# Performance work log

Hardware: AMD Instinct MI355X
Metric: run time of the kernel (lower is better)

Reference implementation:

```python
import jax, jax.numpy as jnp
import numpy as np

MAX_SEQ = 768  # hardcoded in original compute_freqs_cis
THETA = 10000.0


def _freqs_cis(C, T):
    # freqs over FULL embed dim C (matches original, not per-head)
    freqs = 1.0 / THETA ** (jnp.arange(0, C, 2, dtype=jnp.float32)[: C // 2] / C)
    t = jnp.arange(MAX_SEQ, dtype=jnp.float32)
    ang = jnp.outer(t, freqs)  # [MAX_SEQ, C/2]
    return jnp.cos(ang)[:T], jnp.sin(ang)[:T]  # each [T, C/2]


def _apply_rope(u):
    # u: [B, T, C]; rotate adjacent channel pairs across full C
    B, T, C = u.shape
    fr, fi = _freqs_cis(C, T)           # [T, C/2]
    u2 = u.astype(jnp.float32).reshape(B, T, C // 2, 2)
    ur, ui = u2[..., 0], u2[..., 1]     # [B, T, C/2]
    out_r = ur * fr - ui * fi
    out_i = ur * fi + ui * fr
    return jnp.stack([out_r, out_i], axis=-1).reshape(B, T, C).astype(u.dtype)


def setup_inputs() -> dict:
    key = jax.random.key(0)
    k1, k2, k3 = jax.random.split(key, 3)
    B, T, C = 16, 768, 1024
    x = jax.random.normal(k1, (B, T, C), dtype=jnp.float32)
    Wqkv = jax.random.normal(k2, (3 * C, C), dtype=jnp.float32) * 0.02
    bqkv = jnp.zeros((3 * C,), dtype=jnp.float32)
    Wo = jax.random.normal(k3, (C, C), dtype=jnp.float32) * 0.02
    bo = jnp.zeros((C,), dtype=jnp.float32)
    return {"x": x, "Wqkv": Wqkv, "bqkv": bqkv, "Wo": Wo, "bo": bo}


def reference(x, Wqkv, bqkv, Wo, bo):
    B, T, C = x.shape
    H = 16
    D = C // H
    qkv = x @ Wqkv.T + bqkv                      # [B, T, 3C]
    q, k, v = jnp.split(qkv, 3, axis=-1)
    q = _apply_rope(q)
    k = _apply_rope(k)
    # [B, H, T, D]
    q = q.reshape(B, T, H, D).transpose(0, 2, 1, 3)
    k = k.reshape(B, T, H, D).transpose(0, 2, 1, 3)
    v = v.reshape(B, T, H, D).transpose(0, 2, 1, 3)
    scale = 1.0 / jnp.sqrt(jnp.asarray(D, dtype=q.dtype))
    scores = jnp.einsum("bhqd,bhkd->bhqk", q, k) * scale
    causal = jnp.tril(jnp.ones((T, T), dtype=bool))
    scores = jnp.where(causal, scores, jnp.finfo(scores.dtype).min)
    attn = jax.nn.softmax(scores, axis=-1)
    y = jnp.einsum("bhqk,bhkd->bhqd", attn, v)   # [B, H, T, D]
    y = y.transpose(0, 2, 1, 3).reshape(B, T, C)
    return y @ Wo.T + bo
```

## Files before the change

### kernel.cpp

```cpp
#include <hip/hip_runtime.h>
#include <hip/hip_bf16.h>

typedef __attribute__((ext_vector_type(8))) short bf16x8;
typedef __attribute__((ext_vector_type(4))) float f32x4;
typedef unsigned short u16;
typedef unsigned int u32;

#define DEV __device__ __forceinline__

DEV float bf2f(u16 v) { u32 u = ((u32)v) << 16; return __builtin_bit_cast(float, u); }
DEV u16 f2bf(float f) {
    u32 u = __builtin_bit_cast(u32, f);
    u32 r = (u + 0x7FFFu + ((u >> 16) & 1u)) >> 16;
    return (u16)r;
}
DEV u16 f2bf_trunc(float f) { return (u16)(__builtin_bit_cast(u32, f) >> 16); }

DEV void gll16(const u16* g, u16* l) {
    __builtin_amdgcn_global_load_lds((const __attribute__((address_space(1))) void*)g,
                                     (__attribute__((address_space(3))) void*)l, 16, 0, 0);
}

#define WAIT_VM0()   asm volatile("s_waitcnt vmcnt(0)" ::: "memory")
#define WAIT_LGKM0() asm volatile("s_waitcnt lgkmcnt(0)" ::: "memory")
#define BAR()        __builtin_amdgcn_s_barrier()
#define BARF()       asm volatile("s_barrier" ::: "memory")

__global__ void detect_kernel(const u32* __restrict__ x, int* __restrict__ flag) {
    __shared__ int cnt;
    if (threadIdx.x == 0) cnt = 0;
    __syncthreads();
    int c = 0;
    for (int i = threadIdx.x; i < 4096; i += 256) {
        u32 w = x[i];
        u32 e = (w >> 7) & 0xFF;
        c += (e >= 110 && e <= 132) ? 1 : 0;
    }
    atomicAdd(&cnt, c);
    __syncthreads();
    if (threadIdx.x == 0) *flag = (cnt * 2 > 4096) ? 1 : 0;
}

DEV void cvt8(const void* in, u16* out, int i, int fl) {
    if (fl) {
        ((bf16x8*)out)[i] = ((const bf16x8*)in)[i];
    } else {
        float4 a = ((const float4*)in)[2 * i], b = ((const float4*)in)[2 * i + 1];
        bf16x8 o;
        o[0] = (short)f2bf(a.x); o[1] = (short)f2bf(a.y);
        o[2] = (short)f2bf(a.z); o[3] = (short)f2bf(a.w);
        o[4] = (short)f2bf(b.x); o[5] = (short)f2bf(b.y);
        o[6] = (short)f2bf(b.z); o[7] = (short)f2bf(b.w);
        ((bf16x8*)out)[i] = o;
    }
}

__global__ void prep_kernel(const void* __restrict__ x, u16* __restrict__ xb,
                            const void* __restrict__ Wq, u16* __restrict__ Wqb,
                            const void* __restrict__ Wo, u16* __restrict__ Wob,
                            float2* __restrict__ tab, const int* __restrict__ flag) {
    constexpr int N8X = 1572864, N8W = 393216, N8O = 131072;
    constexpr int C1 = N8X, C2 = N8X + N8W, C3 = N8X + N8W + N8O;
    constexpr int TOTAL = C3 + 768 * 512;
    const int fl = *flag;
    const int stride = gridDim.x * 256;
    for (int i = blockIdx.x * 256 + threadIdx.x; i < TOTAL; i += stride) {
        if (i < C1)       cvt8(x, xb, i, fl);
        else if (i < C2)  cvt8(Wq, Wqb, i - C1, fl);
        else if (i < C3)  cvt8(Wo, Wob, i - C2, fl);
        else {
            int r = i - C3;
            int t = r >> 9, j = r & 511;
            float freq = expf(-(float)(2 * j) * (9.210340371976184f / 1024.0f));
            float ang = (float)t * freq;
            tab[r] = make_float2(cosf(ang), sinf(ang));
        }
    }
}

template<int BN>
__global__ __launch_bounds__(512, 2)
void gemm256p_kernel(const u16* __restrict__ A, const u16* __restrict__ W,
                     const void* __restrict__ bias, void* __restrict__ C,
                     int N, const int* __restrict__ flag, int out_mode,
                     const float2* __restrict__ tab, int rope) {
    constexpr int K = 1024, NT = 16;
    constexpr int NF = BN / 64;
    __shared__ u16 lds[2][16384 + BN * 64];
    const int tid = threadIdx.x;
    const int l = tid & 63, w = tid >> 6;
    const int wm = w >> 2, wn = w & 3;
    const int lo = l & 15, hi = l >> 4;

    const int M0 = blockIdx.x * 256, N0 = blockIdx.y * BN;

    const int rS = tid >> 3;
    const int qS = (tid & 7) ^ (rS & 7);
    const u16* Ag = A + (size_t)(M0 + rS) * K + qS * 8;
    const u16* Wg = W + (size_t)(N0 + rS) * K + qS * 8;
    const int lb = w * 512;

    f32x4 acc[8][NF] = {};

#define STG_A(kt, slot, half)                                                  \
    {                                                                          \
        u16* sA_ = &lds[slot][(half) * 8192];                                  \
        const u16* ga_ = Ag + (kt) * 64 + (size_t)(128 * (half)) * K;          \
        gll16(ga_,                  sA_ + lb);                                 \
        gll16(ga_ + (size_t)64 * K, sA_ + 4096 + lb);                          \
    }
#define STG_B(kt, slot, half)                                                  \
    {                                                                          \
        u16* sB_ = &lds[slot][16384 + (half) * 8192];                          \
        const u16* gb_ = Wg + (kt) * 64 + (size_t)(128 * (half)) * K;          \
        gll16(gb_,                  sB_ + lb);                                 \
        gll16(gb_ + (size_t)64 * K, sB_ + 4096 + lb);                          \
    }
#define STG_B_ALL(kt, slot)                                                    \
    { STG_B(kt, slot, 0); if (BN == 256) STG_B(kt, slot, 1); }

    STG_A(0, 0, 0); STG_A(0, 0, 1);
    STG_B_ALL(0, 0);
    WAIT_VM0();
    BARF();

    const int csw = lo & 7;

#pragma unroll 1
    for (int t = 0; t < NT; ++t) {
        const int cur = t & 1, nxt = cur ^ 1;
        const u16* sA = &lds[cur][0];
        const u16* sB = &lds[cur][16384];
        bf16x8 afr[4], bfr[NF];

#pragma unroll
        for (int n = 0; n < NF; ++n)
            bfr[n] = *(const bf16x8*)&sB[(wn * (BN / 4) + n * 16 + lo) * 64 + ((hi ^ csw) * 8)];
#pragma unroll
        for (int m = 0; m < 4; ++m)
            afr[m] = *(const bf16x8*)&sA[(wm * 128 + m * 16 + lo) * 64 + ((hi ^ csw) * 8)];
        if (t + 1 < NT) { STG_A(t + 1, nxt, 0); STG_A(t + 1, nxt, 1); }
        BARF();
        __builtin_amdgcn_s_setprio(1);
#pragma unroll
        for (int m = 0; m < 4; ++m)
#pragma unroll
            for (int n = 0; n < NF; ++n)
                acc[m][n] = __builtin_amdgcn_mfma_f32_16x16x32_bf16(afr[m], bfr[n], acc[m][n], 0, 0, 0);
        __builtin_amdgcn_s_setprio(0);
        BARF();

#pragma unroll
        for (int m = 0; m < 4; ++m)
            afr[m] = *(const bf16x8*)&sA[(wm * 128 + 64 + m * 16 + lo) * 64 + ((hi ^ csw) * 8)];
        if (t + 1 < NT) { STG_B_ALL(t + 1, nxt); }
        BARF();
        __builtin_amdgcn_s_setprio(1);
#pragma unroll
        for (int m = 0; m < 4; ++m)
#pragma unroll
            for (int n = 0; n < NF; ++n)
                acc[4 + m][n] = __builtin_amdgcn_mfma_f32_16x16x32_bf16(afr[m], bfr[n], acc[4 + m][n], 0, 0, 0);
        __builtin_amdgcn_s_setprio(0);
        BARF();

#pragma unroll
        for (int n = 0; n < NF; ++n)
            bfr[n] = *(const bf16x8*)&sB[(wn * (BN / 4) + n * 16 + lo) * 64 + (((4 + hi) ^ csw) * 8)];
#pragma unroll
        for (int m = 0; m < 4; ++m)
            afr[m] = *(const bf16x8*)&sA[(wm * 128 + m * 16 + lo) * 64 + (((4 + hi) ^ csw) * 8)];
        BARF();
        __builtin_amdgcn_s_setprio(1);
#pragma unroll
        for (int m = 0; m < 4; ++m)
#pragma unroll
            for (int n = 0; n < NF; ++n)
                acc[m][n] = __builtin_amdgcn_mfma_f32_16x16x32_bf16(afr[m], bfr[n], acc[m][n], 0, 0, 0);
        __builtin_amdgcn_s_setprio(0);
        BARF();

#pragma unroll
        for (int m = 0; m < 4; ++m)
            afr[m] = *(const bf16x8*)&sA[(wm * 128 + 64 + m * 16 + lo) * 64 + (((4 + hi) ^ csw) * 8)];
        WAIT_VM0();
        BARF();
        __builtin_amdgcn_s_setprio(1);
#pragma unroll
        for (int m = 0; m < 4; ++m)
#pragma unroll
            for (int n = 0; n < NF; ++n)
                acc[4 + m][n] = __builtin_amdgcn_mfma_f32_16x16x32_bf16(afr[m], bfr[n], acc[4 + m][n], 0, 0, 0);
        __builtin_amdgcn_s_setprio(0);
        BARF();
    }
#undef STG_A
#undef STG_B
#undef STG_B_ALL

    const int fl = *flag;
    const int f32out = out_mode ? (fl == 0) : 0;
    const int do_rope = rope && (N0 < 2048);
#pragma unroll
    for (int mi = 0; mi < 8; ++mi) {
        const int rbase = M0 + wm * 128 + (mi >> 2) * 64 + (mi & 3) * 16 + hi * 4;
        const int tbase = (M0 % 768) + wm * 128 + (mi >> 2) * 64 + (mi & 3) * 16 + hi * 4;
#pragma unroll
        for (int n = 0; n < NF; ++n) {
            const int col = N0 + wn * (BN / 4) + lo + n * 16;
            float bi = fl ? bf2f(((const u16*)bias)[col]) : ((const float*)bias)[col];
            const int jf = (col & 1023) >> 1;
            const int odd = col & 1;
#pragma unroll
            for (int j = 0; j < 4; ++j) {
                float v = acc[mi][n][j] + bi;
                if (do_rope) {
                    float partner = __shfl_xor(v, 1);
                    float2 cs = tab[(tbase + j) * 512 + jf];
                    v = odd ? (v * cs.x + partner * cs.y) : (v * cs.x - partner * cs.y);
                }
                size_t idx = (size_t)(rbase + j) * N + col;
                if (f32out) ((float*)C)[idx] = v;
                else        ((u16*)C)[idx] = f2bf(v);
            }
        }
    }
}

__global__ __launch_bounds__(512)
void attn_kernel(const u16* __restrict__ qkv, u16* __restrict__ y) {
    constexpr int T = 768, CH = 1024, QKVC = 3072;
    constexpr float NEG = -30000.0f;
    __shared__ u16 Ks[2][64 * 64];
    __shared__ u16 Vt[64 * 72];
    __shared__ u16 Ps[128 * 72];

    const int tid = threadIdx.x, l = tid & 63, w = tid >> 6;
    const int qt = blockIdx.x, h = blockIdx.y, b = blockIdx.z;
    const int lo = l & 15, hi = l >> 4;
    const int kk = hi * 8;
    const int swzk = (lo & 7) * 8;

    const int qrow = qt * 128 + w * 16 + lo;
    const u16* qptr = qkv + (size_t)(b * T + qrow) * QKVC + h * 64 + kk;
    bf16x8 aq0r = *(const bf16x8*)qptr;
    bf16x8 aq1r = *(const bf16x8*)(qptr + 32);
    bf16x8 aq0, aq1;
#pragma unroll
    for (int e = 0; e < 8; ++e) {
        aq0[e] = (short)f2bf(bf2f((u16)aq0r[e]) * 0.125f);
        aq1[e] = (short)f2bf(bf2f((u16)aq1r[e]) * 0.125f);
    }

    f32x4 o[4] = {};
    float mrun[4] = {NEG, NEG, NEG, NEG};
    float lrun[4] = {0.f, 0.f, 0.f, 0.f};

    const int ksr = w * 8 + (l >> 3);
    const int ksc = ((l & 7) ^ ((l >> 3) & 7)) * 8;
    const u16* kbase = qkv + (size_t)(b * T + ksr) * QKVC + CH + h * 64 + ksc;

    const int vd0 = (tid & 7) * 8;
    const int vswz = (tid & 7) * 8;
    const int vr0 = tid >> 3;
    const u16* vbase = qkv + (size_t)(b * T) * QKVC + 2 * CH + h * 64 + vd0;

    const int NTk = 2 * qt + 2;

    gll16(kbase, &Ks[0][w * 512]);
    bf16x8 cv0 = *(const bf16x8*)(vbase + (size_t)vr0 * QKVC);
    WAIT_VM0();
#pragma unroll
    for (int e = 0; e < 8; ++e)
        Vt[(vd0 + e) * 72 + (vr0 ^ vswz)] = (u16)cv0[e];

    for (int kt = 0; kt < NTk; ++kt) {
        const int cur = kt & 1, nxt = cur ^ 1;
        bf16x8 nv0;
        if (kt + 1 < NTk) {
            const size_t koff = (size_t)((kt + 1) * 64) * QKVC;
            gll16(kbase + koff, &Ks[nxt][w * 512]);
            nv0 = *(const bf16x8*)(vbase + (size_t)((kt + 1) * 64 + vr0) * QKVC);
        }
        WAIT_LGKM0();
        BAR();

        __builtin_amdgcn_s_setprio(1);
        f32x4 s[4];
#pragma unroll
        for (int n = 0; n < 4; ++n) {
            bf16x8 kb0 = *(const bf16x8*)&Ks[cur][(n * 16 + lo) * 64 + (kk ^ swzk)];
            bf16x8 kb1 = *(const bf16x8*)&Ks[cur][(n * 16 + lo) * 64 + ((32 + kk) ^ swzk)];
            f32x4 z = {0.f, 0.f, 0.f, 0.f};
            z = __builtin_amdgcn_mfma_f32_16x16x32_bf16(aq0, kb0, z, 0, 0, 0);
            z = __builtin_amdgcn_mfma_f32_16x16x32_bf16(aq1, kb1, z, 0, 0, 0);
            s[n] = z;
        }
        __builtin_amdgcn_s_setprio(0);

        if (kt >= 2 * qt) {
#pragma unroll
            for (int n = 0; n < 4; ++n) {
                int kcol = kt * 64 + n * 16 + lo;
#pragma unroll
                for (int j = 0; j < 4; ++j)
                    if (kcol > qt * 128 + w * 16 + hi * 4 + j) s[n][j] = NEG;
            }
        }
        float mx[4];
#pragma unroll
        for (int j = 0; j < 4; ++j) {
            float m0 = fmaxf(fmaxf(s[0][j], s[1][j]), fmaxf(s[2][j], s[3][j]));
            m0 = fmaxf(m0, __shfl_xor(m0, 1));
            m0 = fmaxf(m0, __shfl_xor(m0, 2));
            m0 = fmaxf(m0, __shfl_xor(m0, 4));
            m0 = fmaxf(m0, __shfl_xor(m0, 8));
            mx[j] = m0;
        }
        float g = fmaxf(fmaxf(mx[0] - mrun[0], mx[1] - mrun[1]),
                        fmaxf(mx[2] - mrun[2], mx[3] - mrun[3]));
        if (!__all(g <= 8.0f)) {
#pragma unroll
            for (int j = 0; j < 4; ++j) {
                float mn = fmaxf(mrun[j], mx[j]);
                float c = __expf(mrun[j] - mn);
                mrun[j] = mn;
                lrun[j] *= c;
#pragma unroll
                for (int n = 0; n < 4; ++n) o[n][j] *= c;
            }
        }
        float p[4][4];
#pragma unroll
        for (int n = 0; n < 4; ++n)
#pragma unroll
            for (int j = 0; j < 4; ++j) {
                p[n][j] = __expf(s[n][j] - mrun[j]);
                Ps[(w * 16 + hi * 4 + j) * 72 + n * 16 + lo] = f2bf_trunc(p[n][j]);
            }
#pragma unroll
        for (int j = 0; j < 4; ++j)
            lrun[j] += p[0][j] + p[1][j] + p[2][j] + p[3][j];

        __builtin_amdgcn_s_setprio(1);
#pragma unroll
        for (int c = 0; c < 2; ++c) {
            bf16x8 pa = *(const bf16x8*)&Ps[(w * 16 + lo) * 72 + c * 32 + kk];
#pragma unroll
            for (int n = 0; n < 4; ++n) {
                const int v = (n * 2 + (lo >> 3)) & 7;
                bf16x8 vb = *(const bf16x8*)&Vt[(n * 16 + lo) * 72 + ((c * 32 + kk) ^ (v * 8))];
                o[n] = __builtin_amdgcn_mfma_f32_16x16x32_bf16(pa, vb, o[n], 0, 0, 0);
            }
        }
        __builtin_amdgcn_s_setprio(0);

        if (kt + 1 < NTk) {
            WAIT_VM0();
            BAR();
#pragma unroll
            for (int e = 0; e < 8; ++e)
                Vt[(vd0 + e) * 72 + (vr0 ^ vswz)] = (u16)nv0[e];
        }
    }

    float inv[4];
#pragma unroll
    for (int j = 0; j < 4; ++j) {
        float r = lrun[j];
        r += __shfl_xor(r, 1);
        r += __shfl_xor(r, 2);
        r += __shfl_xor(r, 4);
        r += __shfl_xor(r, 8);
        inv[j] = (r > 0.f) ? 1.0f / r : 0.f;
    }
#pragma unroll
    for (int n = 0; n < 4; ++n)
#pragma unroll
        for (int j = 0; j < 4; ++j) {
            int t = qt * 128 + w * 16 + hi * 4 + j;
            y[(size_t)(b * T + t) * CH + h * 64 + n * 16 + lo] = f2bf(o[n][j] * inv[j]);
        }
}

extern "C" void kernel_launch(void* const* d_in, const int* in_sizes, int n_in,
                              void* d_out, int out_size, void* d_ws, size_t ws_size,
                              hipStream_t stream) {
    char* ws = (char*)d_ws;
    int*   flag  = (int*)ws;
    u16*   xb    = (u16*)(ws + 256);
    u16*   Wqb   = (u16*)(ws + 256 + 25165824);
    u16*   Wob   = (u16*)(ws + 256 + 31457280);
    u16*   qkv   = (u16*)(ws + 256 + 33570816);
    u16*   y     = (u16*)(ws + 256 + 109068288);
    float2* tab  = (float2*)(ws + 256 + 134234112);

    detect_kernel<<<1, 256, 0, stream>>>((const u32*)d_in[0], flag);
    prep_kernel<<<2048, 256, 0, stream>>>(d_in[0], xb, d_in[1], Wqb, d_in[3], Wob, tab, flag);

    gemm256p_kernel<256><<<dim3(48, 12), 512, 0, stream>>>(xb, Wqb, d_in[2], qkv, 3072, flag, 0, tab, 1);
    attn_kernel<<<dim3(6, 16, 16), 512, 0, stream>>>(qkv, y);
    gemm256p_kernel<128><<<dim3(48, 8), 512, 0, stream>>>(y, Wob, d_in[4], d_out, 1024, flag, 1, tab, 0);
}
```

Measured before the change: 294.7 us.

## Halve GEMM K-tile to 32 with smaller LDS and fold dtype detection into prep

The GEMM K-step tile drops from 64 to 32. That halves the LDS footprint per stage, possibly allowing more resident blocks, but doubles the number of pipeline iterations and barriers. The staging loads, the swizzle pattern and the per-iteration schedule are rewritten to match, with one fused stage and a wait before the second MFMA half. The separate dtype-detection kernel is also removed: every prep block now recomputes the detection flag itself, saving one launch at the cost of redundant reads.

Result: no change. 295.2 us (+0.2%).

```diff
diff --git a/kernel.cpp b/kernel.cpp
--- a/kernel.cpp
+++ b/kernel.cpp
@@ -25,21 +25,6 @@
 #define WAIT_LGKM0() asm volatile("s_waitcnt lgkmcnt(0)" ::: "memory")
 #define BAR()        __builtin_amdgcn_s_barrier()
 #define BARF()       asm volatile("s_barrier" ::: "memory")
-
-__global__ void detect_kernel(const u32* __restrict__ x, int* __restrict__ flag) {
-    __shared__ int cnt;
-    if (threadIdx.x == 0) cnt = 0;
-    __syncthreads();
-    int c = 0;
-    for (int i = threadIdx.x; i < 4096; i += 256) {
-        u32 w = x[i];
-        u32 e = (w >> 7) & 0xFF;
-        c += (e >= 110 && e <= 132) ? 1 : 0;
-    }
-    atomicAdd(&cnt, c);
-    __syncthreads();
-    if (threadIdx.x == 0) *flag = (cnt * 2 > 4096) ? 1 : 0;
-}
 
 DEV void cvt8(const void* in, u16* out, int i, int fl) {
     if (fl) {
@@ -58,11 +43,26 @@
 __global__ void prep_kernel(const void* __restrict__ x, u16* __restrict__ xb,
                             const void* __restrict__ Wq, u16* __restrict__ Wqb,
                             const void* __restrict__ Wo, u16* __restrict__ Wob,
-                            float2* __restrict__ tab, const int* __restrict__ flag) {
+                            float2* __restrict__ tab, int* __restrict__ flag) {
+    __shared__ int cnt;
+    if (threadIdx.x == 0) cnt = 0;
+    __syncthreads();
+    {
+        int c = 0;
+        for (int i = threadIdx.x; i < 4096; i += 256) {
+            u32 w = ((const u32*)x)[i];
+            u32 e = (w >> 7) & 0xFF;
+            c += (e >= 110 && e <= 132) ? 1 : 0;
+        }
+        atomicAdd(&cnt, c);
+    }
+    __syncthreads();
+    const int fl = (cnt * 2 > 4096) ? 1 : 0;
+    if (blockIdx.x == 0 && threadIdx.x == 0) *flag = fl;
+
     constexpr int N8X = 1572864, N8W = 393216, N8O = 131072;
     constexpr int C1 = N8X, C2 = N8X + N8W, C3 = N8X + N8W + N8O;
     constexpr int TOTAL = C3 + 768 * 512;
-    const int fl = *flag;
     const int stride = gridDim.x * 256;
     for (int i = blockIdx.x * 256 + threadIdx.x; i < TOTAL; i += stride) {
         if (i < C1)       cvt8(x, xb, i, fl);
@@ -84,9 +84,9 @@
                      const void* __restrict__ bias, void* __restrict__ C,
                      int N, const int* __restrict__ flag, int out_mode,
                      const float2* __restrict__ tab, int rope) {
-    constexpr int K = 1024, NT = 16;
+    constexpr int K = 1024, NT = 32;
     constexpr int NF = BN / 64;
-    __shared__ u16 lds[2][16384 + BN * 64];
+    __shared__ u16 lds[2][8192 + BN * 32];
     const int tid = threadIdx.x;
     const int l = tid & 63, w = tid >> 6;
     const int wm = w >> 2, wn = w & 3;
@@ -94,52 +94,46 @@
 
     const int M0 = blockIdx.x * 256, N0 = blockIdx.y * BN;
 
-    const int rS = tid >> 3;
-    const int qS = (tid & 7) ^ (rS & 7);
+    const int rS = tid >> 2;
+    const int qS = (tid & 3) ^ ((tid >> 3) & 3);
     const u16* Ag = A + (size_t)(M0 + rS) * K + qS * 8;
     const u16* Wg = W + (size_t)(N0 + rS) * K + qS * 8;
     const int lb = w * 512;
 
     f32x4 acc[8][NF] = {};
 
-#define STG_A(kt, slot, half)                                                  \
+#define STAGE(kt, slot)                                                        \
     {                                                                          \
-        u16* sA_ = &lds[slot][(half) * 8192];                                  \
-        const u16* ga_ = Ag + (kt) * 64 + (size_t)(128 * (half)) * K;          \
-        gll16(ga_,                  sA_ + lb);                                 \
-        gll16(ga_ + (size_t)64 * K, sA_ + 4096 + lb);                          \
-    }
-#define STG_B(kt, slot, half)                                                  \
-    {                                                                          \
-        u16* sB_ = &lds[slot][16384 + (half) * 8192];                          \
-        const u16* gb_ = Wg + (kt) * 64 + (size_t)(128 * (half)) * K;          \
-        gll16(gb_,                  sB_ + lb);                                 \
-        gll16(gb_ + (size_t)64 * K, sB_ + 4096 + lb);                          \
-    }
-#define STG_B_ALL(kt, slot)                                                    \
-    { STG_B(kt, slot, 0); if (BN == 256) STG_B(kt, slot, 1); }
-
-    STG_A(0, 0, 0); STG_A(0, 0, 1);
-    STG_B_ALL(0, 0);
+        u16* sA_ = &lds[slot][0];                                              \
+        u16* sB_ = &lds[slot][8192];                                           \
+        const u16* ga_ = Ag + (kt) * 32;                                       \
+        const u16* gb_ = Wg + (kt) * 32;                                       \
+        gll16(ga_,                   sA_ + lb);                                \
+        gll16(ga_ + (size_t)128 * K, sA_ + 4096 + lb);                         \
+        gll16(gb_,                   sB_ + lb);                                \
+        if (BN == 256) gll16(gb_ + (size_t)128 * K, sB_ + 4096 + lb);          \
+    }
+
+    STAGE(0, 0);
     WAIT_VM0();
     BARF();
 
-    const int csw = lo & 7;
+    const int csw = (lo & 7) >> 1;
 
 #pragma unroll 1
     for (int t = 0; t < NT; ++t) {
         const int cur = t & 1, nxt = cur ^ 1;
         const u16* sA = &lds[cur][0];
-        const u16* sB = &lds[cur][16384];
+        const u16* sB = &lds[cur][8192];
         bf16x8 afr[4], bfr[NF];
 
 #pragma unroll
         for (int n = 0; n < NF; ++n)
-            bfr[n] = *(const bf16x8*)&sB[(wn * (BN / 4) + n * 16 + lo) * 64 + ((hi ^ csw) * 8)];
+            bfr[n] = *(const bf16x8*)&sB[(wn * (BN / 4) + n * 16 + lo) * 32 + ((hi ^ csw) * 8)];
 #pragma unroll
         for (int m = 0; m < 4; ++m)
-            afr[m] = *(const bf16x8*)&sA[(wm * 128 + m * 16 + lo) * 64 + ((hi ^ csw) * 8)];
-        if (t + 1 < NT) { STG_A(t + 1, nxt, 0); STG_A(t + 1, nxt, 1); }
+            afr[m] = *(const bf16x8*)&sA[(wm * 128 + m * 16 + lo) * 32 + ((hi ^ csw) * 8)];
+        if (t + 1 < NT) STAGE(t + 1, nxt);
         BARF();
         __builtin_amdgcn_s_setprio(1);
 #pragma unroll
@@ -152,8 +146,8 @@
 
 #pragma unroll
         for (int m = 0; m < 4; ++m)
-            afr[m] = *(const bf16x8*)&sA[(wm * 128 + 64 + m * 16 + lo) * 64 + ((hi ^ csw) * 8)];
-        if (t + 1 < NT) { STG_B_ALL(t + 1, nxt); }
+            afr[m] = *(const bf16x8*)&sA[(wm * 128 + 64 + m * 16 + lo) * 32 + ((hi ^ csw) * 8)];
+        if (t + 1 < NT) WAIT_VM0();
         BARF();
         __builtin_amdgcn_s_setprio(1);
 #pragma unroll
@@ -163,40 +157,8 @@
                 acc[4 + m][n] = __builtin_amdgcn_mfma_f32_16x16x32_bf16(afr[m], bfr[n], acc[4 + m][n], 0, 0, 0);
         __builtin_amdgcn_s_setprio(0);
         BARF();
-
-#pragma unroll
-        for (int n = 0; n < NF; ++n)
-            bfr[n] = *(const bf16x8*)&sB[(wn * (BN / 4) + n * 16 + lo) * 64 + (((4 + hi) ^ csw) * 8)];
-#pragma unroll
-        for (int m = 0; m < 4; ++m)
-            afr[m] = *(const bf16x8*)&sA[(wm * 128 + m * 16 + lo) * 64 + (((4 + hi) ^ csw) * 8)];
-        BARF();
-        __builtin_amdgcn_s_setprio(1);
-#pragma unroll
-        for (int m = 0; m < 4; ++m)
-#pragma unroll
-            for (int n = 0; n < NF; ++n)
-                acc[m][n] = __builtin_amdgcn_mfma_f32_16x16x32_bf16(afr[m], bfr[n], acc[m][n], 0, 0, 0);
-        __builtin_amdgcn_s_setprio(0);
-        BARF();
-
-#pragma unroll
-        for (int m = 0; m < 4; ++m)
-            afr[m] = *(const bf16x8*)&sA[(wm * 128 + 64 + m * 16 + lo) * 64 + (((4 + hi) ^ csw) * 8)];
-        WAIT_VM0();
-        BARF();
-        __builtin_amdgcn_s_setprio(1);
-#pragma unroll
-        for (int m = 0; m < 4; ++m)
-#pragma unroll
-            for (int n = 0; n < NF; ++n)
-                acc[4 + m][n] = __builtin_amdgcn_mfma_f32_16x16x32_bf16(afr[m], bfr[n], acc[4 + m][n], 0, 0, 0);
-        __builtin_amdgcn_s_setprio(0);
-        BARF();
-    }
-#undef STG_A
-#undef STG_B
-#undef STG_B_ALL
+    }
+#undef STAGE
 
     const int fl = *flag;
     const int f32out = out_mode ? (fl == 0) : 0;
@@ -395,7 +357,6 @@
     u16*   y     = (u16*)(ws + 256 + 109068288);
     float2* tab  = (float2*)(ws + 256 + 134234112);
 
-    detect_kernel<<<1, 256, 0, stream>>>((const u32*)d_in[0], flag);
     prep_kernel<<<2048, 256, 0, stream>>>(d_in[0], xb, d_in[1], Wqb, d_in[3], Wob, tab, flag);
 
     gemm256p_kernel<256><<<dim3(48, 12), 512, 0, stream>>>(xb, Wqb, d_in[2], qkv, 3072, flag, 0, tab, 1);
```
